# Kernel optimization log

Measured on AMD Instinct MI355X. Metric: run time of the kernel, lower is better.

The kernel has to match this reference:

```python
import jax, jax.numpy as jnp
import numpy as np

B, N, D, H, K = 16, 256, 64, 64, 2  # batch, nodes, d_in, d_hidden, top_k


def setup_inputs() -> dict:
    key = jax.random.key(0)
    k0, k1, k2 = jax.random.split(key, 3)
    O = jax.random.normal(k0, (B, N, D), dtype=jnp.float32)
    # PairwiseFeaturizer.proj: Linear(4*D, H) -> ReLU -> Linear(H, 1)
    W1 = jax.random.normal(k1, (4 * D, H), dtype=jnp.float32) / np.sqrt(4 * D).astype(np.float32)
    b1 = jnp.zeros((H,), dtype=jnp.float32)
    W2 = jax.random.normal(k2, (H, 1), dtype=jnp.float32) / np.sqrt(H).astype(np.float32)
    b2 = jnp.zeros((1,), dtype=jnp.float32)
    return {"O": O, "W1": W1, "b1": b1, "W2": W2, "b2": b2}


def reference(O, W1, b1, W2, b2):
    Bn, Nn, d = O.shape
    ii, jj = jnp.triu_indices(Nn, k=1)  # all undirected pairs i<j, M = N(N-1)/2
    Oi = O[:, ii, :]  # (B, M, d) gather
    Oj = O[:, jj, :]  # (B, M, d) gather
    feats = jnp.concatenate([Oi, Oj, jnp.abs(Oi - Oj), Oi * Oj], axis=-1)  # (B, M, 4d)
    h = jax.nn.relu(jnp.einsum('bmf,fh->bmh', feats, W1) + b1)
    Q = (jnp.einsum('bmh,ho->bmo', h, W2) + b2)[..., 0]  # (B, M)
    # greedy top-k selection mask (eps -> 0 limit of select_pairs)
    idx = jax.lax.top_k(Q, K)[1]  # (B, K)
    mask = jnp.zeros(Q.shape, dtype=bool).at[jnp.arange(Q.shape[0])[:, None], idx].set(True)
    return Q, mask
```

## Files before the change

kernel.cpp:

```cpp
#include <hip/hip_runtime.h>
#include <math.h>

#define Bn 16
#define Nn 256
#define Dd 64
#define Mm (Nn*(Nn-1)/2)
#define NT 8
#define CHUNK 4080

typedef __attribute__((ext_vector_type(8))) short bf16x8;
typedef __attribute__((ext_vector_type(4))) short short4v;
typedef __attribute__((ext_vector_type(4))) float f32x4;

typedef union { bf16x8 v; short s[8]; __bf16 h[8]; } F8;
typedef union { short4v v; __bf16 h[4]; } F4;

#define MFMA(acc, a, b) \
  acc = __builtin_amdgcn_mfma_f32_16x16x32_bf16((a), (b), (acc), 0, 0, 0)

__device__ __forceinline__ void top2_update(float v, int m,
    float& v1, int& i1, float& v2, int& i2)
{
  bool c1 = (v > v1) || (v == v1 && m < i1);
  bool c2 = (v > v2) || (v == v2 && m < i2);
  float nv2 = c1 ? v1 : (c2 ? v : v2);
  int   ni2 = c1 ? i1 : (c2 ? m : i2);
  v1 = c1 ? v : v1;  i1 = c1 ? m : i1;
  v2 = nv2;          i2 = ni2;
}

__global__ __launch_bounds__(256, 2) void pair_kernel(
    const float* __restrict__ O,
    const float* __restrict__ W1,
    const float* __restrict__ b1,
    const float* __restrict__ W2,
    const float* __restrict__ b2,
    float* __restrict__ Q,
    float* __restrict__ cand)
{
  __shared__ __align__(16) unsigned short wt[64][264];
  __shared__ __align__(16) unsigned short s_oi[32][72];
  __shared__ __align__(16) unsigned short s_oj[32][72];
  __shared__ float s_AT[64][33];
  __shared__ float s_CT[64][33];
  __shared__ float s_q [32][36];
  __shared__ float s_red[4][4];

  const int t  = threadIdx.x;
  const int l  = t & 63, wv = t >> 6;
  const int lo = l & 15, g = l >> 4;

  const int blk   = blockIdx.x;
  const int batch = blk / 36;
  int tile        = blk % 36;
  int a = 0;
  while (tile >= (NT - a)) { tile -= NT - a; ++a; }
  const int ti0 = a * 32, tj0 = (a + tile) * 32;
  const bool diag = (tile == 0);

  const float* Ob = O + (size_t)batch * Nn * Dd;

  {
    const float4* Oi4 = (const float4*)(Ob + ti0 * Dd);
    const float4* Oj4 = (const float4*)(Ob + tj0 * Dd);
    #pragma unroll
    for (int p = 0; p < 2; ++p) {
      int v = t + p * 256;
      int r = v >> 4, c4 = (v & 15) * 4;
      float4 x = Oi4[v];
      F4 ai; ai.h[0] = (__bf16)x.x; ai.h[1] = (__bf16)x.y;
             ai.h[2] = (__bf16)x.z; ai.h[3] = (__bf16)x.w;
      *(short4v*)&s_oi[r][c4] = ai.v;
      float4 y = Oj4[v];
      F4 aj; aj.h[0] = (__bf16)y.x; aj.h[1] = (__bf16)y.y;
             aj.h[2] = (__bf16)y.z; aj.h[3] = (__bf16)y.w;
      *(short4v*)&s_oj[r][c4] = aj.v;
    }
  }
  {
    #pragma unroll
    for (int it = 0; it < 8; ++it) {
      int h  = t & 63;
      int gq = (t >> 6) + 4 * it;
      int k0 = gq * 8;
      F8 wk;
      #pragma unroll
      for (int e = 0; e < 8; ++e)
        wk.h[e] = (__bf16)W1[(k0 + e) * 64 + h];
      *(bf16x8*)&wt[h][k0] = wk.v;
    }
  }
  __syncthreads();

  {
    const int  mf  = wv & 1;
    const bool isA = (wv < 2);
    const int  bk  = isA ? 0 : 64;
    const unsigned short (*src)[72] = isA ? s_oi : s_oj;

    F8 bf[2][4];
    #pragma unroll
    for (int ks = 0; ks < 2; ++ks)
      #pragma unroll
      for (int nf = 0; nf < 4; ++nf)
        bf[ks][nf].v = *(const bf16x8*)&wt[nf * 16 + lo][bk + ks * 32 + g * 8];

    F8 aop[2];
    #pragma unroll
    for (int ks = 0; ks < 2; ++ks)
      aop[ks].v = *(const bf16x8*)&src[mf * 16 + lo][ks * 32 + g * 8];

    f32x4 ac0 = {0.f,0.f,0.f,0.f}, ac1 = {0.f,0.f,0.f,0.f},
          ac2 = {0.f,0.f,0.f,0.f}, ac3 = {0.f,0.f,0.f,0.f};
    #pragma unroll
    for (int ks = 0; ks < 2; ++ks) {
      MFMA(ac0, aop[ks].v, bf[ks][0].v);
      MFMA(ac1, aop[ks].v, bf[ks][1].v);
      MFMA(ac2, aop[ks].v, bf[ks][2].v);
      MFMA(ac3, aop[ks].v, bf[ks][3].v);
    }

    float bad0 = 0.f, bad1 = 0.f, bad2 = 0.f, bad3 = 0.f;
    if (isA) {
      bad0 = b1[lo]; bad1 = b1[16 + lo]; bad2 = b1[32 + lo]; bad3 = b1[48 + lo];
    }
    float (*dst)[33] = isA ? s_AT : s_CT;
    const int rbase = mf * 16 + g * 4;
    #pragma unroll
    for (int r = 0; r < 4; ++r) {
      dst[lo     ][rbase + r] = ac0[r] + bad0;
      dst[16 + lo][rbase + r] = ac1[r] + bad1;
      dst[32 + lo][rbase + r] = ac2[r] + bad2;
      dst[48 + lo][rbase + r] = ac3[r] + bad3;
    }
  }
  __syncthreads();

  F8 bfr[4][4];
  #pragma unroll
  for (int ks = 0; ks < 4; ++ks)
    #pragma unroll
    for (int nf = 0; nf < 4; ++nf)
      bfr[ks][nf].v = *(const bf16x8*)&wt[nf * 16 + lo][128 + ks * 32 + g * 8];

  float ojv[2][16];
  #pragma unroll
  for (int jh = 0; jh < 2; ++jh) {
    F8 u0, u1;
    u0.v = *(const bf16x8*)&s_oj[jh * 16 + lo][g * 8];
    u1.v = *(const bf16x8*)&s_oj[jh * 16 + lo][32 + g * 8];
    #pragma unroll
    for (int e = 0; e < 8; ++e) {
      ojv[jh][e]     = (float)u0.h[e];
      ojv[jh][8 + e] = (float)u1.h[e];
    }
  }

  float cin[2][4][4];
  #pragma unroll
  for (int jh = 0; jh < 2; ++jh)
    #pragma unroll
    for (int nf = 0; nf < 4; ++nf)
      #pragma unroll
      for (int r = 0; r < 4; ++r)
        cin[jh][nf][r] = s_CT[nf * 16 + lo][jh * 16 + g * 4 + r];

  float w2v[4] = { W2[lo], W2[16 + lo], W2[32 + lo], W2[48 + lo] };

  for (int ii = 0; ii < 8; ++ii) {
    const int iL = wv * 8 + ii;
    float oiv[16];
    {
      F8 u0, u1;
      u0.v = *(const bf16x8*)&s_oi[iL][g * 8];
      u1.v = *(const bf16x8*)&s_oi[iL][32 + g * 8];
      #pragma unroll
      for (int e = 0; e < 8; ++e) {
        oiv[e]     = (float)u0.h[e];
        oiv[8 + e] = (float)u1.h[e];
      }
    }
    float ah[4] = { s_AT[lo][iL], s_AT[16 + lo][iL],
                    s_AT[32 + lo][iL], s_AT[48 + lo][iL] };

    #pragma unroll
    for (int jh = 0; jh < 2; ++jh) {
      f32x4 acc0, acc1, acc2, acc3;
      #pragma unroll
      for (int r = 0; r < 4; ++r) {
        acc0[r] = cin[jh][0][r] + ah[0];
        acc1[r] = cin[jh][1][r] + ah[1];
        acc2[r] = cin[jh][2][r] + ah[2];
        acc3[r] = cin[jh][3][r] + ah[3];
      }

      F8 a0, a1, a2, a3;
      #pragma unroll
      for (int e = 0; e < 8; ++e) {
        float p0 = ojv[jh][e], p1 = ojv[jh][8 + e];
        a0.h[e] = (__bf16)fabsf(oiv[e]     - p0);
        a1.h[e] = (__bf16)fabsf(oiv[8 + e] - p1);
        a2.h[e] = (__bf16)(oiv[e]     * p0);
        a3.h[e] = (__bf16)(oiv[8 + e] * p1);
      }
      MFMA(acc0, a0.v, bfr[0][0].v); MFMA(acc1, a0.v, bfr[0][1].v);
      MFMA(acc2, a0.v, bfr[0][2].v); MFMA(acc3, a0.v, bfr[0][3].v);
      MFMA(acc0, a1.v, bfr[1][0].v); MFMA(acc1, a1.v, bfr[1][1].v);
      MFMA(acc2, a1.v, bfr[1][2].v); MFMA(acc3, a1.v, bfr[1][3].v);
      MFMA(acc0, a2.v, bfr[2][0].v); MFMA(acc1, a2.v, bfr[2][1].v);
      MFMA(acc2, a2.v, bfr[2][2].v); MFMA(acc3, a2.v, bfr[2][3].v);
      MFMA(acc0, a3.v, bfr[3][0].v); MFMA(acc1, a3.v, bfr[3][1].v);
      MFMA(acc2, a3.v, bfr[3][2].v); MFMA(acc3, a3.v, bfr[3][3].v);

      float val0, val1, val2, val3;
      val0 = fmaxf(acc0[0], 0.f) * w2v[0] + fmaxf(acc1[0], 0.f) * w2v[1]
           + fmaxf(acc2[0], 0.f) * w2v[2] + fmaxf(acc3[0], 0.f) * w2v[3];
      val1 = fmaxf(acc0[1], 0.f) * w2v[0] + fmaxf(acc1[1], 0.f) * w2v[1]
           + fmaxf(acc2[1], 0.f) * w2v[2] + fmaxf(acc3[1], 0.f) * w2v[3];
      val2 = fmaxf(acc0[2], 0.f) * w2v[0] + fmaxf(acc1[2], 0.f) * w2v[1]
           + fmaxf(acc2[2], 0.f) * w2v[2] + fmaxf(acc3[2], 0.f) * w2v[3];
      val3 = fmaxf(acc0[3], 0.f) * w2v[0] + fmaxf(acc1[3], 0.f) * w2v[1]
           + fmaxf(acc2[3], 0.f) * w2v[2] + fmaxf(acc3[3], 0.f) * w2v[3];
      #pragma unroll
      for (int s = 1; s < 16; s <<= 1) {
        val0 += __shfl_xor(val0, s, 16);
        val1 += __shfl_xor(val1, s, 16);
        val2 += __shfl_xor(val2, s, 16);
        val3 += __shfl_xor(val3, s, 16);
      }
      float sel = val0;
      sel = (lo == 1) ? val1 : sel;
      sel = (lo == 2) ? val2 : sel;
      sel = (lo == 3) ? val3 : sel;
      if (lo < 4) s_q[iL][jh * 16 + g * 4 + lo] = sel;
    }
  }
  __syncthreads();

  {
    const float b2v = b2[0];
    const int row = t >> 3, c4 = (t & 7) * 4;
    const int i = ti0 + row;
    float4 q4 = *(const float4*)&s_q[row][c4];
    const int K0 = i * (Nn - 1) - (i * (i - 1)) / 2 + tj0 + c4 - i - 1;
    float v1 = -INFINITY, v2 = -INFINITY;
    int   i1 = 0x7fffffff, i2 = 0x7fffffff;
    float qe[4] = { q4.x + b2v, q4.y + b2v, q4.z + b2v, q4.w + b2v };
    #pragma unroll
    for (int e = 0; e < 4; ++e) {
      int j = tj0 + c4 + e;
      bool valid = !diag || (j > i);
      if (valid) {
        Q[(size_t)batch * Mm + K0 + e] = qe[e];
        top2_update(qe[e], K0 + e, v1, i1, v2, i2);
      }
    }
    #pragma unroll
    for (int s = 1; s < 64; s <<= 1) {
      float u1 = __shfl_xor(v1, s); int j1 = __shfl_xor(i1, s);
      float u2 = __shfl_xor(v2, s); int j2 = __shfl_xor(i2, s);
      top2_update(u1, j1, v1, i1, v2, i2);
      top2_update(u2, j2, v1, i1, v2, i2);
    }
    if (l == 0) {
      s_red[wv][0] = v1; s_red[wv][1] = __int_as_float(i1);
      s_red[wv][2] = v2; s_red[wv][3] = __int_as_float(i2);
    }
    __syncthreads();
    if (t == 0) {
      float a1 = s_red[0][0]; int x1 = __float_as_int(s_red[0][1]);
      float a2 = s_red[0][2]; int x2 = __float_as_int(s_red[0][3]);
      #pragma unroll
      for (int e = 1; e < 4; ++e) {
        top2_update(s_red[e][0], __float_as_int(s_red[e][1]), a1, x1, a2, x2);
        top2_update(s_red[e][2], __float_as_int(s_red[e][3]), a1, x1, a2, x2);
      }
      float* cp = cand + (size_t)blk * 4;
      cp[0] = a1; cp[1] = __int_as_float(x1);
      cp[2] = a2; cp[3] = __int_as_float(x2);
    }
  }
}

__global__ __launch_bounds__(256) void rank_kernel(
    const float* __restrict__ O, const float* __restrict__ W1,
    const float* __restrict__ b1, const float* __restrict__ W2,
    const float* __restrict__ cand, int* __restrict__ ws2)
{
  const int b = blockIdx.x;
  const int t = threadIdx.x;
  __shared__ float s_cv[72];
  __shared__ int   s_ci[72];
  __shared__ int   s_m[8];
  __shared__ int   s_ij[8][2];
  __shared__ float s_or[8][2][64];
  __shared__ float s_part[8][32];
  __shared__ float s_qe[8];

  if (t < 72) {
    const float* cp = cand + (size_t)(b * 36 + (t >> 1)) * 4;
    s_cv[t] = cp[(t & 1) * 2];
    s_ci[t] = __float_as_int(cp[(t & 1) * 2 + 1]);
  }
  __syncthreads();
  if (t < 72) {
    float v = s_cv[t]; int m = s_ci[t];
    int rank = 0;
    for (int e = 0; e < 72; ++e) {
      float u = s_cv[e]; int n = s_ci[e];
      rank += (u > v || (u == v && n < m)) ? 1 : 0;
    }
    if (rank < 8) s_m[rank] = m;
  }
  __syncthreads();
  if (t < 16) {
    int m = s_m[t >> 1];
    int i = 0, rem = m;
    while (rem >= Nn - 1 - i) { rem -= Nn - 1 - i; ++i; }
    int j = i + 1 + rem;
    s_ij[t >> 1][t & 1] = (t & 1) ? j : i;
  }
  __syncthreads();
  {
    int c = t >> 5, rr = (t >> 4) & 1, c4 = (t & 15) * 4;
    int row = s_ij[c][rr];
    *(float4*)&s_or[c][rr][c4] = *(const float4*)&O[((size_t)b * Nn + row) * Dd + c4];
  }
  __syncthreads();
  {
    int c = t >> 5, hh = t & 31, h2 = hh * 2;
    float z0 = b1[h2], z1 = b1[h2 + 1];
    for (int d = 0; d < 64; ++d) {
      float oi = s_or[c][0][d], oj = s_or[c][1][d];
      float f3 = fabsf(oi - oj), f4 = oi * oj;
      float2 wa = *(const float2*)&W1[(d      ) * 64 + h2];
      float2 wb = *(const float2*)&W1[(64 + d ) * 64 + h2];
      float2 wc = *(const float2*)&W1[(128 + d) * 64 + h2];
      float2 wd = *(const float2*)&W1[(192 + d) * 64 + h2];
      z0 += oi * wa.x + oj * wb.x + f3 * wc.x + f4 * wd.x;
      z1 += oi * wa.y + oj * wb.y + f3 * wc.y + f4 * wd.y;
    }
    s_part[c][hh] = fmaxf(z0, 0.f) * W2[h2] + fmaxf(z1, 0.f) * W2[h2 + 1];
  }
  __syncthreads();
  if (t < 8) {
    float s = 0.f;
    for (int e = 0; e < 32; ++e) s += s_part[t][e];
    s_qe[t] = s;
  }
  __syncthreads();
  if (t == 0) {
    float v1 = -INFINITY, v2 = -INFINITY;
    int   i1 = 0x7fffffff, i2 = 0x7fffffff;
    for (int e = 0; e < 8; ++e)
      top2_update(s_qe[e], s_m[e], v1, i1, v2, i2);
    ws2[b * 2] = i1; ws2[b * 2 + 1] = i2;
  }
}

__global__ __launch_bounds__(256) void mask_kernel(
    const int* __restrict__ ws2, float* __restrict__ mask)
{
  const int b = blockIdx.x >> 3, cch = blockIdx.x & 7, t = threadIdx.x;
  const int k0 = ws2[b * 2], k1 = ws2[b * 2 + 1];
  float* mb = mask + (size_t)b * Mm;
  const int m0 = cch * CHUNK;
  for (int m = m0 + t; m < m0 + CHUNK; m += 256)
    mb[m] = (m == k0 || m == k1) ? 1.0f : 0.0f;
}

extern "C" void kernel_launch(void* const* d_in, const int* in_sizes, int n_in,
                              void* d_out, int out_size, void* d_ws, size_t ws_size,
                              hipStream_t stream) {
  const float* O  = (const float*)d_in[0];
  const float* W1 = (const float*)d_in[1];
  const float* b1 = (const float*)d_in[2];
  const float* W2 = (const float*)d_in[3];
  const float* b2 = (const float*)d_in[4];

  float* Q    = (float*)d_out;
  float* mask = Q + (size_t)Bn * Mm;
  float* cand = (float*)d_ws;
  int*   ws2  = (int*)d_ws + 4096;

  pair_kernel<<<dim3(Bn * 36), dim3(256), 0, stream>>>(O, W1, b1, W2, b2, Q, cand);
  rank_kernel<<<dim3(Bn), dim3(256), 0, stream>>>(O, W1, b1, W2, cand, ws2);
  mask_kernel<<<dim3(Bn * 8), dim3(256), 0, stream>>>(ws2, mask);
}
```

Baseline: 59.75 us.

## Pretranspose W1 in a prep kernel and halve pair tiles to 16x32

A new prep kernel converts W1 once to a transposed bf16 copy in global memory, so each pair block no longer rebuilds a 33KB LDS weight tile. Pair blocks read MFMA weight operands straight from global memory or cache instead. Tiles shrink to 16 i-rows by 32 j-columns, which doubles the block count to 1152 and cuts LDS use so three blocks can fit per CU. The MFMA operand order is swapped so the W2 reduction needs only two cross-lane shuffles. The price is an extra kernel launch, twice as many candidates for rank_kernel to sort, and more global-load traffic for weights.

Measured after the change: 59.45 us. About the same (-0.5%).

```diff
diff --git a/kernel.cpp b/kernel.cpp
--- a/kernel.cpp
+++ b/kernel.cpp
@@ -3,9 +3,7 @@
 
 #define Bn 16
 #define Nn 256
-#define Dd 64
 #define Mm (Nn*(Nn-1)/2)
-#define NT 8
 #define CHUNK 4080
 
 typedef __attribute__((ext_vector_type(8))) short bf16x8;
@@ -29,21 +27,30 @@
   v2 = nv2;          i2 = ni2;
 }
 
-__global__ __launch_bounds__(256, 2) void pair_kernel(
+__global__ __launch_bounds__(256) void prep_w1t(
+    const float* __restrict__ W1, unsigned short* __restrict__ wtg)
+{
+  const int h = blockIdx.x;
+  const int k = threadIdx.x;
+  __bf16 b = (__bf16)W1[k * 64 + h];
+  wtg[h * 256 + k] = *(unsigned short*)&b;
+}
+
+__global__ __launch_bounds__(256, 3) void pair_kernel(
     const float* __restrict__ O,
-    const float* __restrict__ W1,
     const float* __restrict__ b1,
     const float* __restrict__ W2,
     const float* __restrict__ b2,
+    const unsigned short* __restrict__ wtg,
     float* __restrict__ Q,
     float* __restrict__ cand)
 {
-  __shared__ __align__(16) unsigned short wt[64][264];
-  __shared__ __align__(16) unsigned short s_oi[32][72];
+  __shared__ __align__(16) unsigned short s_oi[16][72];
   __shared__ __align__(16) unsigned short s_oj[32][72];
-  __shared__ float s_AT[64][33];
-  __shared__ float s_CT[64][33];
-  __shared__ float s_q [32][36];
+  __shared__ float s_A[16][68];
+  __shared__ float s_C[32][68];
+  __shared__ float s_q[16][36];
+  __shared__ float s_w2[64];
   __shared__ float s_red[4][4];
 
   const int t  = threadIdx.x;
@@ -51,124 +58,88 @@
   const int lo = l & 15, g = l >> 4;
 
   const int blk   = blockIdx.x;
-  const int batch = blk / 36;
-  int tile        = blk % 36;
+  const int batch = blk / 72;
+  int tl          = blk % 72;
   int a = 0;
-  while (tile >= (NT - a)) { tile -= NT - a; ++a; }
-  const int ti0 = a * 32, tj0 = (a + tile) * 32;
-  const bool diag = (tile == 0);
-
-  const float* Ob = O + (size_t)batch * Nn * Dd;
+  while (tl >= 8 - (a >> 1)) { tl -= 8 - (a >> 1); ++a; }
+  const int c   = (a >> 1) + tl;
+  const int ti0 = a * 16, tj0 = c * 32;
+
+  const float* Ob = O + (size_t)batch * Nn * 64;
 
   {
-    const float4* Oi4 = (const float4*)(Ob + ti0 * Dd);
-    const float4* Oj4 = (const float4*)(Ob + tj0 * Dd);
-    #pragma unroll
-    for (int p = 0; p < 2; ++p) {
-      int v = t + p * 256;
+    const float4* Oi4 = (const float4*)(Ob + ti0 * 64);
+    {
+      int r = t >> 4, c4 = (t & 15) * 4;
+      float4 x = Oi4[t];
+      F4 p; p.h[0] = (__bf16)x.x; p.h[1] = (__bf16)x.y;
+            p.h[2] = (__bf16)x.z; p.h[3] = (__bf16)x.w;
+      *(short4v*)&s_oi[r][c4] = p.v;
+    }
+    const float4* Oj4 = (const float4*)(Ob + tj0 * 64);
+    #pragma unroll
+    for (int p2 = 0; p2 < 2; ++p2) {
+      int v = t + p2 * 256;
       int r = v >> 4, c4 = (v & 15) * 4;
-      float4 x = Oi4[v];
-      F4 ai; ai.h[0] = (__bf16)x.x; ai.h[1] = (__bf16)x.y;
-             ai.h[2] = (__bf16)x.z; ai.h[3] = (__bf16)x.w;
-      *(short4v*)&s_oi[r][c4] = ai.v;
-      float4 y = Oj4[v];
-      F4 aj; aj.h[0] = (__bf16)y.x; aj.h[1] = (__bf16)y.y;
-             aj.h[2] = (__bf16)y.z; aj.h[3] = (__bf16)y.w;
-      *(short4v*)&s_oj[r][c4] = aj.v;
-    }
-  }
-  {
-    #pragma unroll
-    for (int it = 0; it < 8; ++it) {
-      int h  = t & 63;
-      int gq = (t >> 6) + 4 * it;
-      int k0 = gq * 8;
-      F8 wk;
-      #pragma unroll
-      for (int e = 0; e < 8; ++e)
-        wk.h[e] = (__bf16)W1[(k0 + e) * 64 + h];
-      *(bf16x8*)&wt[h][k0] = wk.v;
-    }
-  }
-  __syncthreads();
-
-  {
-    const int  mf  = wv & 1;
-    const bool isA = (wv < 2);
-    const int  bk  = isA ? 0 : 64;
-    const unsigned short (*src)[72] = isA ? s_oi : s_oj;
-
-    F8 bf[2][4];
-    #pragma unroll
-    for (int ks = 0; ks < 2; ++ks)
-      #pragma unroll
-      for (int nf = 0; nf < 4; ++nf)
-        bf[ks][nf].v = *(const bf16x8*)&wt[nf * 16 + lo][bk + ks * 32 + g * 8];
-
-    F8 aop[2];
-    #pragma unroll
-    for (int ks = 0; ks < 2; ++ks)
-      aop[ks].v = *(const bf16x8*)&src[mf * 16 + lo][ks * 32 + g * 8];
-
-    f32x4 ac0 = {0.f,0.f,0.f,0.f}, ac1 = {0.f,0.f,0.f,0.f},
-          ac2 = {0.f,0.f,0.f,0.f}, ac3 = {0.f,0.f,0.f,0.f};
-    #pragma unroll
-    for (int ks = 0; ks < 2; ++ks) {
-      MFMA(ac0, aop[ks].v, bf[ks][0].v);
-      MFMA(ac1, aop[ks].v, bf[ks][1].v);
-      MFMA(ac2, aop[ks].v, bf[ks][2].v);
-      MFMA(ac3, aop[ks].v, bf[ks][3].v);
-    }
-
-    float bad0 = 0.f, bad1 = 0.f, bad2 = 0.f, bad3 = 0.f;
-    if (isA) {
-      bad0 = b1[lo]; bad1 = b1[16 + lo]; bad2 = b1[32 + lo]; bad3 = b1[48 + lo];
-    }
-    float (*dst)[33] = isA ? s_AT : s_CT;
-    const int rbase = mf * 16 + g * 4;
-    #pragma unroll
-    for (int r = 0; r < 4; ++r) {
-      dst[lo     ][rbase + r] = ac0[r] + bad0;
-      dst[16 + lo][rbase + r] = ac1[r] + bad1;
-      dst[32 + lo][rbase + r] = ac2[r] + bad2;
-      dst[48 + lo][rbase + r] = ac3[r] + bad3;
-    }
-  }
-  __syncthreads();
+      float4 x = Oj4[v];
+      F4 p; p.h[0] = (__bf16)x.x; p.h[1] = (__bf16)x.y;
+            p.h[2] = (__bf16)x.z; p.h[3] = (__bf16)x.w;
+      *(short4v*)&s_oj[r][c4] = p.v;
+    }
+    if (t < 64) s_w2[t] = W2[t];
+  }
+  __syncthreads();
+
+  if (wv < 2) {
+    #pragma unroll
+    for (int nn = 0; nn < 2; ++nn) {
+      const int nf = wv * 2 + nn;
+      f32x4 ac = {0.f, 0.f, 0.f, 0.f};
+      #pragma unroll
+      for (int ks = 0; ks < 2; ++ks) {
+        F8 aop; aop.v = *(const bf16x8*)&s_oi[lo][ks * 32 + g * 8];
+        F8 bop; bop.v = *(const bf16x8*)&wtg[(nf * 16 + lo) * 256 + ks * 32 + g * 8];
+        MFMA(ac, aop.v, bop.v);
+      }
+      const float bb = b1[nf * 16 + lo];
+      #pragma unroll
+      for (int r = 0; r < 4; ++r)
+        s_A[g * 4 + r][nf * 16 + lo] = ac[r] + bb;
+    }
+  } else {
+    const int mf = wv - 2;
+    #pragma unroll
+    for (int nf = 0; nf < 4; ++nf) {
+      f32x4 ac = {0.f, 0.f, 0.f, 0.f};
+      #pragma unroll
+      for (int ks = 0; ks < 2; ++ks) {
+        F8 aop; aop.v = *(const bf16x8*)&s_oj[mf * 16 + lo][ks * 32 + g * 8];
+        F8 bop; bop.v = *(const bf16x8*)&wtg[(nf * 16 + lo) * 256 + 64 + ks * 32 + g * 8];
+        MFMA(ac, aop.v, bop.v);
+      }
+      #pragma unroll
+      for (int r = 0; r < 4; ++r)
+        s_C[mf * 16 + g * 4 + r][nf * 16 + lo] = ac[r];
+    }
+  }
 
   F8 bfr[4][4];
   #pragma unroll
   for (int ks = 0; ks < 4; ++ks)
     #pragma unroll
     for (int nf = 0; nf < 4; ++nf)
-      bfr[ks][nf].v = *(const bf16x8*)&wt[nf * 16 + lo][128 + ks * 32 + g * 8];
-
-  float ojv[2][16];
-  #pragma unroll
-  for (int jh = 0; jh < 2; ++jh) {
-    F8 u0, u1;
-    u0.v = *(const bf16x8*)&s_oj[jh * 16 + lo][g * 8];
-    u1.v = *(const bf16x8*)&s_oj[jh * 16 + lo][32 + g * 8];
-    #pragma unroll
-    for (int e = 0; e < 8; ++e) {
-      ojv[jh][e]     = (float)u0.h[e];
-      ojv[jh][8 + e] = (float)u1.h[e];
-    }
-  }
-
-  float cin[2][4][4];
-  #pragma unroll
-  for (int jh = 0; jh < 2; ++jh)
+      bfr[ks][nf].v = *(const bf16x8*)&wtg[(nf * 16 + lo) * 256 + 128 + ks * 32 + g * 8];
+
+  __syncthreads();
+
+  for (int ii = 0; ii < 4; ++ii) {
+    const int iL = wv * 4 + ii;
+
+    f32x4 as4[4];
     #pragma unroll
     for (int nf = 0; nf < 4; ++nf)
-      #pragma unroll
-      for (int r = 0; r < 4; ++r)
-        cin[jh][nf][r] = s_CT[nf * 16 + lo][jh * 16 + g * 4 + r];
-
-  float w2v[4] = { W2[lo], W2[16 + lo], W2[32 + lo], W2[48 + lo] };
-
-  for (int ii = 0; ii < 8; ++ii) {
-    const int iL = wv * 8 + ii;
+      as4[nf] = *(const f32x4*)&s_A[iL][nf * 16 + g * 4];
+
     float oiv[16];
     {
       F8 u0, u1;
@@ -180,79 +151,82 @@
         oiv[8 + e] = (float)u1.h[e];
       }
     }
-    float ah[4] = { s_AT[lo][iL], s_AT[16 + lo][iL],
-                    s_AT[32 + lo][iL], s_AT[48 + lo][iL] };
 
     #pragma unroll
     for (int jh = 0; jh < 2; ++jh) {
+      F8 fb0, fb1, fb2, fb3;
+      {
+        F8 v0, v1;
+        v0.v = *(const bf16x8*)&s_oj[jh * 16 + lo][g * 8];
+        v1.v = *(const bf16x8*)&s_oj[jh * 16 + lo][32 + g * 8];
+        #pragma unroll
+        for (int e = 0; e < 8; ++e) {
+          float p0 = (float)v0.h[e], p1 = (float)v1.h[e];
+          float d0 = oiv[e] - p0,    d1 = oiv[8 + e] - p1;
+          fb0.h[e] = (__bf16)fabsf(d0);
+          fb1.h[e] = (__bf16)fabsf(d1);
+          fb2.h[e] = (__bf16)(oiv[e] * p0);
+          fb3.h[e] = (__bf16)(oiv[8 + e] * p1);
+        }
+      }
+
       f32x4 acc0, acc1, acc2, acc3;
-      #pragma unroll
-      for (int r = 0; r < 4; ++r) {
-        acc0[r] = cin[jh][0][r] + ah[0];
-        acc1[r] = cin[jh][1][r] + ah[1];
-        acc2[r] = cin[jh][2][r] + ah[2];
-        acc3[r] = cin[jh][3][r] + ah[3];
-      }
-
-      F8 a0, a1, a2, a3;
-      #pragma unroll
-      for (int e = 0; e < 8; ++e) {
-        float p0 = ojv[jh][e], p1 = ojv[jh][8 + e];
-        a0.h[e] = (__bf16)fabsf(oiv[e]     - p0);
-        a1.h[e] = (__bf16)fabsf(oiv[8 + e] - p1);
-        a2.h[e] = (__bf16)(oiv[e]     * p0);
-        a3.h[e] = (__bf16)(oiv[8 + e] * p1);
-      }
-      MFMA(acc0, a0.v, bfr[0][0].v); MFMA(acc1, a0.v, bfr[0][1].v);
-      MFMA(acc2, a0.v, bfr[0][2].v); MFMA(acc3, a0.v, bfr[0][3].v);
-      MFMA(acc0, a1.v, bfr[1][0].v); MFMA(acc1, a1.v, bfr[1][1].v);
-      MFMA(acc2, a1.v, bfr[1][2].v); MFMA(acc3, a1.v, bfr[1][3].v);
-      MFMA(acc0, a2.v, bfr[2][0].v); MFMA(acc1, a2.v, bfr[2][1].v);
-      MFMA(acc2, a2.v, bfr[2][2].v); MFMA(acc3, a2.v, bfr[2][3].v);
-      MFMA(acc0, a3.v, bfr[3][0].v); MFMA(acc1, a3.v, bfr[3][1].v);
-      MFMA(acc2, a3.v, bfr[3][2].v); MFMA(acc3, a3.v, bfr[3][3].v);
-
-      float val0, val1, val2, val3;
-      val0 = fmaxf(acc0[0], 0.f) * w2v[0] + fmaxf(acc1[0], 0.f) * w2v[1]
-           + fmaxf(acc2[0], 0.f) * w2v[2] + fmaxf(acc3[0], 0.f) * w2v[3];
-      val1 = fmaxf(acc0[1], 0.f) * w2v[0] + fmaxf(acc1[1], 0.f) * w2v[1]
-           + fmaxf(acc2[1], 0.f) * w2v[2] + fmaxf(acc3[1], 0.f) * w2v[3];
-      val2 = fmaxf(acc0[2], 0.f) * w2v[0] + fmaxf(acc1[2], 0.f) * w2v[1]
-           + fmaxf(acc2[2], 0.f) * w2v[2] + fmaxf(acc3[2], 0.f) * w2v[3];
-      val3 = fmaxf(acc0[3], 0.f) * w2v[0] + fmaxf(acc1[3], 0.f) * w2v[1]
-           + fmaxf(acc2[3], 0.f) * w2v[2] + fmaxf(acc3[3], 0.f) * w2v[3];
-      #pragma unroll
-      for (int s = 1; s < 16; s <<= 1) {
-        val0 += __shfl_xor(val0, s, 16);
-        val1 += __shfl_xor(val1, s, 16);
-        val2 += __shfl_xor(val2, s, 16);
-        val3 += __shfl_xor(val3, s, 16);
-      }
-      float sel = val0;
-      sel = (lo == 1) ? val1 : sel;
-      sel = (lo == 2) ? val2 : sel;
-      sel = (lo == 3) ? val3 : sel;
-      if (lo < 4) s_q[iL][jh * 16 + g * 4 + lo] = sel;
+      {
+        f32x4 c0 = *(const f32x4*)&s_C[jh * 16 + lo][0 * 16 + g * 4];
+        f32x4 c1 = *(const f32x4*)&s_C[jh * 16 + lo][1 * 16 + g * 4];
+        f32x4 c2 = *(const f32x4*)&s_C[jh * 16 + lo][2 * 16 + g * 4];
+        f32x4 c3 = *(const f32x4*)&s_C[jh * 16 + lo][3 * 16 + g * 4];
+        acc0 = as4[0] + c0; acc1 = as4[1] + c1;
+        acc2 = as4[2] + c2; acc3 = as4[3] + c3;
+      }
+
+      MFMA(acc0, bfr[0][0].v, fb0.v); MFMA(acc1, bfr[0][1].v, fb0.v);
+      MFMA(acc2, bfr[0][2].v, fb0.v); MFMA(acc3, bfr[0][3].v, fb0.v);
+      MFMA(acc0, bfr[1][0].v, fb1.v); MFMA(acc1, bfr[1][1].v, fb1.v);
+      MFMA(acc2, bfr[1][2].v, fb1.v); MFMA(acc3, bfr[1][3].v, fb1.v);
+      MFMA(acc0, bfr[2][0].v, fb2.v); MFMA(acc1, bfr[2][1].v, fb2.v);
+      MFMA(acc2, bfr[2][2].v, fb2.v); MFMA(acc3, bfr[2][3].v, fb2.v);
+      MFMA(acc0, bfr[3][0].v, fb3.v); MFMA(acc1, bfr[3][1].v, fb3.v);
+      MFMA(acc2, bfr[3][2].v, fb3.v); MFMA(acc3, bfr[3][3].v, fb3.v);
+
+      float part = 0.f;
+      {
+        f32x4 w0 = *(const f32x4*)&s_w2[0 * 16 + g * 4];
+        f32x4 w1 = *(const f32x4*)&s_w2[1 * 16 + g * 4];
+        f32x4 w2q = *(const f32x4*)&s_w2[2 * 16 + g * 4];
+        f32x4 w3 = *(const f32x4*)&s_w2[3 * 16 + g * 4];
+        #pragma unroll
+        for (int r = 0; r < 4; ++r) {
+          part = fmaf(fmaxf(acc0[r], 0.f), w0[r], part);
+          part = fmaf(fmaxf(acc1[r], 0.f), w1[r], part);
+          part = fmaf(fmaxf(acc2[r], 0.f), w2q[r], part);
+          part = fmaf(fmaxf(acc3[r], 0.f), w3[r], part);
+        }
+      }
+      part += __shfl_xor(part, 16);
+      part += __shfl_xor(part, 32);
+      if (g == 0) s_q[iL][jh * 16 + lo] = part;
     }
   }
   __syncthreads();
 
   {
     const float b2v = b2[0];
-    const int row = t >> 3, c4 = (t & 7) * 4;
+    const int e0 = t * 2;
+    const int row = e0 >> 5, col0 = e0 & 31;
     const int i = ti0 + row;
-    float4 q4 = *(const float4*)&s_q[row][c4];
-    const int K0 = i * (Nn - 1) - (i * (i - 1)) / 2 + tj0 + c4 - i - 1;
     float v1 = -INFINITY, v2 = -INFINITY;
     int   i1 = 0x7fffffff, i2 = 0x7fffffff;
-    float qe[4] = { q4.x + b2v, q4.y + b2v, q4.z + b2v, q4.w + b2v };
-    #pragma unroll
-    for (int e = 0; e < 4; ++e) {
-      int j = tj0 + c4 + e;
-      bool valid = !diag || (j > i);
-      if (valid) {
-        Q[(size_t)batch * Mm + K0 + e] = qe[e];
-        top2_update(qe[e], K0 + e, v1, i1, v2, i2);
+    const int mbase = i * (Nn - 1) - (i * (i - 1)) / 2 - i - 1;
+    #pragma unroll
+    for (int e = 0; e < 2; ++e) {
+      const int col = col0 + e;
+      const int j = tj0 + col;
+      const float qv = s_q[row][col] + b2v;
+      if (j > i) {
+        const int m = mbase + j;
+        Q[(size_t)batch * Mm + m] = qv;
+        top2_update(qv, m, v1, i1, v2, i2);
       }
     }
     #pragma unroll
@@ -289,24 +263,24 @@
 {
   const int b = blockIdx.x;
   const int t = threadIdx.x;
-  __shared__ float s_cv[72];
-  __shared__ int   s_ci[72];
+  __shared__ float s_cv[144];
+  __shared__ int   s_ci[144];
   __shared__ int   s_m[8];
   __shared__ int   s_ij[8][2];
   __shared__ float s_or[8][2][64];
   __shared__ float s_part[8][32];
   __shared__ float s_qe[8];
 
-  if (t < 72) {
-    const float* cp = cand + (size_t)(b * 36 + (t >> 1)) * 4;
+  if (t < 144) {
+    const float* cp = cand + (size_t)(b * 72 + (t >> 1)) * 4;
     s_cv[t] = cp[(t & 1) * 2];
     s_ci[t] = __float_as_int(cp[(t & 1) * 2 + 1]);
   }
   __syncthreads();
-  if (t < 72) {
+  if (t < 144) {
     float v = s_cv[t]; int m = s_ci[t];
     int rank = 0;
-    for (int e = 0; e < 72; ++e) {
+    for (int e = 0; e < 144; ++e) {
       float u = s_cv[e]; int n = s_ci[e];
       rank += (u > v || (u == v && n < m)) ? 1 : 0;
     }
@@ -324,7 +298,7 @@
   {
     int c = t >> 5, rr = (t >> 4) & 1, c4 = (t & 15) * 4;
     int row = s_ij[c][rr];
-    *(float4*)&s_or[c][rr][c4] = *(const float4*)&O[((size_t)b * Nn + row) * Dd + c4];
+    *(float4*)&s_or[c][rr][c4] = *(const float4*)&O[((size_t)b * Nn + row) * 64 + c4];
   }
   __syncthreads();
   {
@@ -380,10 +354,13 @@
 
   float* Q    = (float*)d_out;
   float* mask = Q + (size_t)Bn * Mm;
-  float* cand = (float*)d_ws;
-  int*   ws2  = (int*)d_ws + 4096;
-
-  pair_kernel<<<dim3(Bn * 36), dim3(256), 0, stream>>>(O, W1, b1, W2, b2, Q, cand);
+
+  unsigned short* wtg = (unsigned short*)d_ws;
+  float* cand = (float*)((char*)d_ws + 32768);
+  int*   ws2  = (int*)((char*)d_ws + 32768 + 18432);
+
+  prep_w1t<<<dim3(64), dim3(256), 0, stream>>>(W1, wtg);
+  pair_kernel<<<dim3(Bn * 72), dim3(256), 0, stream>>>(O, b1, W2, b2, wtg, Q, cand);
   rank_kernel<<<dim3(Bn), dim3(256), 0, stream>>>(O, W1, b1, W2, cand, ws2);
   mask_kernel<<<dim3(Bn * 8), dim3(256), 0, stream>>>(ws2, mask);
 }
```
